# Kernel tuning notes

Measured on AMD Instinct MI355X. Metric: run time of the kernel, lower is better.

Reference implementation:

```python
import jax, jax.numpy as jnp
import numpy as np

B, C, IMG, P = 16, 3, 224, 16
L, H, D, DK, DV, M, NC = 4, 12, 768, 768, 768, 3072, 4
N = (IMG // P) ** 2  # 196 patches
S = N + 1            # +CLS
EPS = 1e-5


def _ln_stats(x):
    mu = jnp.mean(x, axis=-1, keepdims=True)
    var = jnp.var(x, axis=-1, keepdims=True)
    return (x - mu) * jax.lax.rsqrt(var + EPS)


def setup_inputs() -> dict:
    key = jax.random.key(0)
    ks = iter(jax.random.split(key, 32))
    g = lambda shape, s=0.02: jax.random.normal(next(ks), shape, jnp.float32) * s
    inp = {
        "x": jax.random.normal(next(ks), (B, C, IMG, IMG), jnp.float32),
        "W_patch": g((D, C, P, P)),
        "b_patch": jnp.zeros((D,), jnp.float32),
        "cls_tok": g((1, 1, D), 1.0),
        "pos_emb": g((1, S, D), 1.0),
        # per-layer stacked params (leading dim L); per-head LN + per-head full-width QKV
        "ln1_g": jnp.ones((L, H, D), jnp.float32),
        "ln1_b": jnp.zeros((L, H, D), jnp.float32),
        "Wq": g((L, H, D, DK)), "bq": jnp.zeros((L, H, DK), jnp.float32),
        "Wk": g((L, H, D, DK)), "bk": jnp.zeros((L, H, DK), jnp.float32),
        "Wv": g((L, H, D, DV)), "bv": jnp.zeros((L, H, DV), jnp.float32),
        "Wo": g((L, H * DK, D)), "bo": jnp.zeros((L, D), jnp.float32),
        "ln2_g": jnp.ones((L, D), jnp.float32),
        "ln2_b": jnp.zeros((L, D), jnp.float32),
        "W1": g((L, D, M)), "b1": jnp.zeros((L, M), jnp.float32),
        "W2": g((L, M, D)), "b2": jnp.zeros((L, D), jnp.float32),
        "lnf_g": jnp.ones((D,), jnp.float32),
        "lnf_b": jnp.zeros((D,), jnp.float32),
        "Wc": g((D, NC)), "bc": jnp.zeros((NC,), jnp.float32),
    }
    return inp


def _vit_forward(x, W_patch, b_patch, cls_tok, pos_emb,
                 ln1_g, ln1_b, Wq, bq, Wk, bk, Wv, bv, Wo, bo,
                 ln2_g, ln2_b, W1, b1, W2, b2, lnf_g, lnf_b, Wc, bc):
    b = x.shape[0]
    hp = IMG // P
    # patch embed: stride==kernel conv as a reshape+einsum; order matches conv flatten (h-major)
    xp = x.reshape(b, C, hp, P, hp, P)
    h = jnp.einsum('bchpwq,dcpq->bhwd', xp, W_patch).reshape(b, N, D) + b_patch
    h = jnp.concatenate([jnp.broadcast_to(cls_tok, (b, 1, D)), h], axis=1) + pos_emb

    scale = jnp.sqrt(jnp.asarray(DK, h.dtype))

    def block(h, p):
        (g1, b1_, wq, bq_, wk, bk_, wv, bv_, wo, bo_, g2, b2_, w1, bb1, w2, bb2) = p
        xn = _ln_stats(h)                                   # [B,S,D] shared stats
        xh = xn[:, None] * g1[None, :, None, :] + b1_[None, :, None, :]  # [B,H,S,D]
        q = jnp.einsum('bhsd,hdk->bhsk', xh, wq) + bq_[None, :, None, :]
        k = jnp.einsum('bhsd,hdk->bhsk', xh, wk) + bk_[None, :, None, :]
        v = jnp.einsum('bhsd,hdk->bhsk', xh, wv) + bv_[None, :, None, :]
        scores = jnp.einsum('bhqd,bhkd->bhqk', q, k) / scale
        probs = jax.nn.softmax(scores, axis=-2)             # quirk: softmax over QUERY axis
        av = jnp.einsum('bhqk,bhkd->bhqd', probs, v)        # [B,H,S,DV]
        cat = jnp.transpose(av, (0, 2, 1, 3)).reshape(b, S, H * DV)
        h = h + cat @ wo + bo_
        xn2 = _ln_stats(h) * g2 + b2_
        hid = jax.nn.gelu(xn2 @ w1 + bb1, approximate=False)
        h = h + hid @ w2 + bb2
        return h, None

    params = (ln1_g, ln1_b, Wq, bq, Wk, bk, Wv, bv, Wo, bo,
              ln2_g, ln2_b, W1, b1, W2, b2)
    h, _ = jax.lax.scan(block, h, params)
    cls = _ln_stats(h[:, 0]) * lnf_g + lnf_b
    return cls @ Wc + bc


def reference(x, W_patch, b_patch, cls_tok, pos_emb,
              ln1_g, ln1_b, Wq, bq, Wk, bk, Wv, bv, Wo, bo,
              ln2_g, ln2_b, W1, b1, W2, b2, lnf_g, lnf_b, Wc, bc):
    return _vit_forward(x, W_patch, b_patch, cls_tok, pos_emb,
                        ln1_g, ln1_b, Wq, bq, Wk, bk, Wv, bv, Wo, bo,
                        ln2_g, ln2_b, W1, b1, W2, b2, lnf_g, lnf_b, Wc, bc)
```

## Files before the change

### kernel.cpp

```cpp
#include <hip/hip_runtime.h>
#include <hip/hip_bf16.h>
#include <math.h>

typedef float f32x4 __attribute__((ext_vector_type(4)));
typedef __bf16 bf16x8 __attribute__((ext_vector_type(8)));

#define EPI_PATCH  0
#define EPI_QKV    1
#define EPI_SCORES 2
#define EPI_AV     3
#define EPI_GELU   4
#define EPI_RESID  5

template<int EPI>
__global__ __launch_bounds__(256)
void gemm_bt(const __hip_bfloat16* __restrict__ Ag,
             const __hip_bfloat16* __restrict__ Bg,
             const int M, const int N, const int K,
             const int lda, const int ldb,
             const long sA, const long sB,
             void* __restrict__ outv,
             const float* __restrict__ bias,
             const float* __restrict__ bias2,
             const int ldo, const float p1)
{
    __shared__ unsigned short As[128][32];
    __shared__ unsigned short Bs[128][32];
    const int tid  = threadIdx.x;
    const int lane = tid & 63;
    const int wave = tid >> 6;
    const int wm = (wave & 1) << 6;
    const int wn = (wave >> 1) << 6;
    const int m0 = blockIdx.y * 128;
    const int n0 = blockIdx.x * 128;
    const int z  = blockIdx.z;
    const __hip_bfloat16* A = Ag + (size_t)z * sA;
    const __hip_bfloat16* B = Bg + (size_t)z * sB;

    f32x4 acc[4][4] = {};

    const int fr = lane & 15;
    const int q8 = (lane >> 4) << 3;
    const int rr = tid >> 2;
    const int kc = (tid & 3) << 3;

    for (int k0 = 0; k0 < K; k0 += 32) {
        #pragma unroll
        for (int i = 0; i < 2; ++i) {
            const int r = rr + (i << 6);
            int ra = m0 + r; ra = (ra < M) ? ra : (M - 1);
            int rb = n0 + r; rb = (rb < N) ? rb : (N - 1);
            const uint4 va = *(const uint4*)(A + (size_t)ra * lda + (k0 + kc));
            const uint4 vb = *(const uint4*)(B + (size_t)rb * ldb + (k0 + kc));
            *(uint4*)(&As[r][kc]) = va;
            *(uint4*)(&Bs[r][kc]) = vb;
        }
        __syncthreads();
        bf16x8 af[4], bfr[4];
        #pragma unroll
        for (int mi = 0; mi < 4; ++mi) {
            af[mi] = *(const bf16x8*)(&As[wm + (mi << 4) + fr][q8]);
        }
        #pragma unroll
        for (int ni = 0; ni < 4; ++ni) {
            bfr[ni] = *(const bf16x8*)(&Bs[wn + (ni << 4) + fr][q8]);
        }
        #pragma unroll
        for (int mi = 0; mi < 4; ++mi) {
            #pragma unroll
            for (int ni = 0; ni < 4; ++ni) {
                acc[mi][ni] = __builtin_amdgcn_mfma_f32_16x16x32_bf16(
                    af[mi], bfr[ni], acc[mi][ni], 0, 0, 0);
            }
        }
        __syncthreads();
    }

    const int q4 = (lane >> 4) << 2;
    #pragma unroll
    for (int mi = 0; mi < 4; ++mi) {
        #pragma unroll
        for (int ni = 0; ni < 4; ++ni) {
            #pragma unroll
            for (int r = 0; r < 4; ++r) {
                const int m = m0 + wm + (mi << 4) + q4 + r;
                const int n = n0 + wn + (ni << 4) + fr;
                if (m < M && n < N) {
                    const float v = acc[mi][ni][r];
                    if (EPI == EPI_PATCH) {
                        float* h = (float*)outv;
                        const int b = m / 196;
                        const int pp = m - b * 196;
                        h[(size_t)(m + b + 1) * 768 + n] =
                            v + bias[n] + bias2[(size_t)(1 + pp) * 768 + n];
                    } else if (EPI == EPI_QKV) {
                        __hip_bfloat16* o = (__hip_bfloat16*)outv;
                        const int b = m / 197, s = m - b * 197;
                        const int hh = n / 768, kq = n - hh * 768;
                        o[((size_t)((b * 12 + hh) * 197 + s)) * 768 + kq] =
                            __float2bfloat16(v + bias[n]);
                    } else if (EPI == EPI_SCORES) {
                        float* o = (float*)outv + (size_t)z * 38809;
                        o[(size_t)m * 197 + n] = v * p1;
                    } else if (EPI == EPI_AV) {
                        __hip_bfloat16* o = (__hip_bfloat16*)outv;
                        const int b = z / 12, hh = z - b * 12;
                        o[(size_t)b * 197 * 9216 + (size_t)m * 9216 + hh * 768 + n] =
                            __float2bfloat16(v);
                    } else if (EPI == EPI_GELU) {
                        __hip_bfloat16* o = (__hip_bfloat16*)outv;
                        const float t = v + bias[n];
                        o[(size_t)m * ldo + n] =
                            __float2bfloat16(0.5f * t * (1.0f + erff(t * 0.70710678118654752f)));
                    } else if (EPI == EPI_RESID) {
                        float* h = (float*)outv;
                        h[(size_t)m * 768 + n] += v + bias[n];
                    }
                }
            }
        }
    }
}

__global__ __launch_bounds__(256)
void ln_rows(const float* __restrict__ h, __hip_bfloat16* __restrict__ xn)
{
    const int r = blockIdx.x;
    const float* x = h + (size_t)r * 768;
    float v[3]; float s = 0.f, sq = 0.f;
    #pragma unroll
    for (int i = 0; i < 3; ++i) {
        v[i] = x[threadIdx.x + i * 256];
        s += v[i]; sq += v[i] * v[i];
    }
    __shared__ float sb[8];
    #pragma unroll
    for (int off = 32; off; off >>= 1) {
        s += __shfl_down(s, off); sq += __shfl_down(sq, off);
    }
    const int w = threadIdx.x >> 6;
    if ((threadIdx.x & 63) == 0) { sb[w] = s; sb[4 + w] = sq; }
    __syncthreads();
    s = sb[0] + sb[1] + sb[2] + sb[3];
    sq = sb[4] + sb[5] + sb[6] + sb[7];
    const float mu = s * (1.f / 768.f);
    const float var = sq * (1.f / 768.f) - mu * mu;
    const float rstd = rsqrtf(var + 1e-5f);
    __hip_bfloat16* o = xn + (size_t)r * 768;
    #pragma unroll
    for (int i = 0; i < 3; ++i) {
        o[threadIdx.x + i * 256] = __float2bfloat16((v[i] - mu) * rstd);
    }
}

__global__ __launch_bounds__(256)
void softmax_q(const float* __restrict__ scores, __hip_bfloat16* __restrict__ probs)
{
    const int z = blockIdx.x;
    const float* sc = scores + (size_t)z * 38809;
    __hip_bfloat16* pr = probs + (size_t)z * 197 * 224;
    const int k = threadIdx.x;
    if (k >= 224) return;
    if (k < 197) {
        float mx = -1e30f;
        for (int q = 0; q < 197; ++q) mx = fmaxf(mx, sc[(size_t)q * 197 + k]);
        float sum = 0.f;
        for (int q = 0; q < 197; ++q) sum += expf(sc[(size_t)q * 197 + k] - mx);
        const float inv = 1.f / sum;
        for (int q = 0; q < 197; ++q) {
            pr[(size_t)q * 224 + k] =
                __float2bfloat16(expf(sc[(size_t)q * 197 + k] - mx) * inv);
        }
    } else {
        const __hip_bfloat16 zz = __float2bfloat16(0.f);
        for (int q = 0; q < 197; ++q) pr[(size_t)q * 224 + k] = zz;
    }
}

__device__ __forceinline__
void tconv_body(const float* __restrict__ src, __hip_bfloat16* __restrict__ dst,
                const int R, const int C,
                const float* __restrict__ gain, const float* __restrict__ bvec,
                float* __restrict__ bias_out, const int r0, const int c0)
{
    __shared__ float tile[32][33];
    __shared__ float pb[8][32];
    const int tx = threadIdx.x & 31, ty = threadIdx.x >> 5;
    float bacc = 0.f;
    #pragma unroll
    for (int i = 0; i < 4; ++i) {
        const int r = r0 + ty + i * 8;
        const float w = src[(size_t)r * C + c0 + tx];
        tile[ty + i * 8][tx] = w * (gain ? gain[r] : 1.f);
        if (bvec) bacc += bvec[r] * w;
    }
    if (bias_out) pb[ty][tx] = bacc;
    __syncthreads();
    #pragma unroll
    for (int i = 0; i < 4; ++i) {
        const int c = c0 + ty + i * 8;
        dst[(size_t)c * R + r0 + tx] = __float2bfloat16(tile[tx][ty + i * 8]);
    }
    if (bias_out && ty == 0) {
        float sum = 0.f;
        #pragma unroll
        for (int j = 0; j < 8; ++j) sum += pb[j][tx];
        atomicAdd(&bias_out[c0 + tx], sum);
    }
}

__global__ __launch_bounds__(256)
void tconv_plain(const float* __restrict__ src, __hip_bfloat16* __restrict__ dst,
                 const int R, const int C, const float* __restrict__ gain,
                 const float* __restrict__ bvec, float* __restrict__ bias_out)
{
    tconv_body(src, dst, R, C, gain, bvec, bias_out, blockIdx.y * 32, blockIdx.x * 32);
}

__global__ __launch_bounds__(256)
void tconv_qkv(const float* __restrict__ Wq, const float* __restrict__ Wk,
               const float* __restrict__ Wv, const float* __restrict__ g1,
               const float* __restrict__ b1, __hip_bfloat16* __restrict__ dst,
               float* __restrict__ bias_out, const int l)
{
    const int zz = blockIdx.z;
    const int proj = zz / 12, hh = zz - proj * 12;
    const float* W = (proj == 0) ? Wq : ((proj == 1) ? Wk : Wv);
    const float* src = W + (size_t)(l * 12 + hh) * 768 * 768;
    const float* g = g1 + (size_t)(l * 12 + hh) * 768;
    const float* bv = b1 + (size_t)(l * 12 + hh) * 768;
    __hip_bfloat16* d = dst + ((size_t)proj * 9216 + (size_t)hh * 768) * 768;
    float* bo = bias_out + proj * 9216 + hh * 768;
    tconv_body(src, d, 768, 768, g, bv, bo, blockIdx.y * 32, blockIdx.x * 32);
}

__global__ __launch_bounds__(256)
void vtrans(const __hip_bfloat16* __restrict__ v, __hip_bfloat16* __restrict__ vt)
{
    const int z = blockIdx.z;
    const __hip_bfloat16* src = v + (size_t)z * 197 * 768;
    __hip_bfloat16* dst = vt + (size_t)z * 768 * 224;
    __shared__ __hip_bfloat16 tile[32][33];
    const int tx = threadIdx.x & 31, ty = threadIdx.x >> 5;
    const int s0 = blockIdx.y * 32, d0 = blockIdx.x * 32;
    #pragma unroll
    for (int i = 0; i < 4; ++i) {
        const int s = s0 + ty + i * 8;
        tile[ty + i * 8][tx] = (s < 197) ? src[(size_t)s * 768 + d0 + tx]
                                         : __float2bfloat16(0.f);
    }
    __syncthreads();
    #pragma unroll
    for (int i = 0; i < 4; ++i) {
        const int d = d0 + ty + i * 8;
        dst[(size_t)d * 224 + s0 + tx] = tile[tx][ty + i * 8];
    }
}

__global__ void im2col_patch(const float* __restrict__ x, __hip_bfloat16* __restrict__ Ap)
{
    const int idx = blockIdx.x * 256 + threadIdx.x;
    if (idx >= 3136 * 768) return;
    const int m = idx / 768, kk = idx - m * 768;
    const int b = m / 196, pidx = m - b * 196;
    const int ph = pidx / 14, pw = pidx - ph * 14;
    const int c = kk >> 8, rrr = kk & 255;
    const int p = rrr >> 4, q = rrr & 15;
    Ap[idx] = __float2bfloat16(
        x[(((size_t)b * 3 + c) * 224 + ph * 16 + p) * 224 + pw * 16 + q]);
}

__global__ void conv_ew(const float* __restrict__ src, __hip_bfloat16* __restrict__ dst, const int n)
{
    const int i = blockIdx.x * 256 + threadIdx.x;
    if (i < n) dst[i] = __float2bfloat16(src[i]);
}

__global__ void cls_pos(const float* __restrict__ cls, const float* __restrict__ pos,
                        float* __restrict__ h)
{
    const int i = blockIdx.x * 256 + threadIdx.x;
    if (i < 16 * 768) {
        const int b = i / 768, d = i - b * 768;
        h[(size_t)b * 197 * 768 + d] = cls[d] + pos[d];
    }
}

__global__ void binit_qkv(const float* __restrict__ bq, const float* __restrict__ bk,
                          const float* __restrict__ bv, float* __restrict__ bias, const int l)
{
    const int n = blockIdx.x * 256 + threadIdx.x;
    if (n < 3 * 9216) {
        const int proj = n / 9216, rem = n - proj * 9216;
        const int hh = rem / 768, kq = rem - hh * 768;
        const float* src = (proj == 0) ? bq : ((proj == 1) ? bk : bv);
        bias[n] = src[(size_t)(l * 12 + hh) * 768 + kq];
    }
}

__global__ void binit_vec(const float* __restrict__ src, float* __restrict__ dst, const int n)
{
    const int i = blockIdx.x * 256 + threadIdx.x;
    if (i < n) dst[i] = src[i];
}

__global__ __launch_bounds__(256)
void final_head(const float* __restrict__ h, const float* __restrict__ lnfg,
                const float* __restrict__ lnfb, const float* __restrict__ Wc,
                const float* __restrict__ bc, float* __restrict__ out)
{
    const int b = blockIdx.x;
    const float* x = h + (size_t)b * 197 * 768;
    float v[3]; float s = 0.f, sq = 0.f;
    #pragma unroll
    for (int i = 0; i < 3; ++i) {
        v[i] = x[threadIdx.x + i * 256];
        s += v[i]; sq += v[i] * v[i];
    }
    __shared__ float sb[8];
    #pragma unroll
    for (int off = 32; off; off >>= 1) {
        s += __shfl_down(s, off); sq += __shfl_down(sq, off);
    }
    const int w = threadIdx.x >> 6;
    if ((threadIdx.x & 63) == 0) { sb[w] = s; sb[4 + w] = sq; }
    __syncthreads();
    s = sb[0] + sb[1] + sb[2] + sb[3];
    sq = sb[4] + sb[5] + sb[6] + sb[7];
    const float mu = s * (1.f / 768.f);
    const float var = sq * (1.f / 768.f) - mu * mu;
    const float rstd = rsqrtf(var + 1e-5f);
    float pacc[4] = {0.f, 0.f, 0.f, 0.f};
    #pragma unroll
    for (int i = 0; i < 3; ++i) {
        const int d = threadIdx.x + i * 256;
        const float c = (v[i] - mu) * rstd * lnfg[d] + lnfb[d];
        #pragma unroll
        for (int n = 0; n < 4; ++n) pacc[n] += c * Wc[d * 4 + n];
    }
    __shared__ float rb[4][4];
    #pragma unroll
    for (int off = 32; off; off >>= 1) {
        #pragma unroll
        for (int n = 0; n < 4; ++n) pacc[n] += __shfl_down(pacc[n], off);
    }
    if ((threadIdx.x & 63) == 0) {
        #pragma unroll
        for (int n = 0; n < 4; ++n) rb[w][n] = pacc[n];
    }
    __syncthreads();
    if (threadIdx.x < 4) {
        out[b * 4 + threadIdx.x] =
            rb[0][threadIdx.x] + rb[1][threadIdx.x] + rb[2][threadIdx.x] +
            rb[3][threadIdx.x] + bc[threadIdx.x];
    }
}

extern "C" void kernel_launch(void* const* d_in, const int* in_sizes, int n_in,
                              void* d_out, int out_size, void* d_ws, size_t ws_size,
                              hipStream_t stream)
{
    const float* x    = (const float*)d_in[0];
    const float* Wp   = (const float*)d_in[1];
    const float* bp   = (const float*)d_in[2];
    const float* cls  = (const float*)d_in[3];
    const float* pos  = (const float*)d_in[4];
    const float* g1   = (const float*)d_in[5];
    const float* b1v  = (const float*)d_in[6];
    const float* Wq   = (const float*)d_in[7];
    const float* bq   = (const float*)d_in[8];
    const float* Wk   = (const float*)d_in[9];
    const float* bk   = (const float*)d_in[10];
    const float* Wv   = (const float*)d_in[11];
    const float* bv   = (const float*)d_in[12];
    const float* Wo   = (const float*)d_in[13];
    const float* bo   = (const float*)d_in[14];
    const float* g2   = (const float*)d_in[15];
    const float* b2v  = (const float*)d_in[16];
    const float* W1   = (const float*)d_in[17];
    const float* bb1  = (const float*)d_in[18];
    const float* W2   = (const float*)d_in[19];
    const float* bb2  = (const float*)d_in[20];
    const float* lnfg = (const float*)d_in[21];
    const float* lnfb = (const float*)d_in[22];
    const float* Wc   = (const float*)d_in[23];
    const float* bc   = (const float*)d_in[24];
    float* out = (float*)d_out;

    char* p = (char*)d_ws;
    auto alloc = [&](size_t bytes) {
        char* r = p; p += (bytes + 255) & ~(size_t)255; return r;
    };
    float*          h       = (float*)         alloc((size_t)3152 * 768 * 4);
    __hip_bfloat16* xn      = (__hip_bfloat16*)alloc((size_t)3152 * 768 * 2);
    __hip_bfloat16* Ap      = (__hip_bfloat16*)alloc((size_t)3136 * 768 * 2);
    __hip_bfloat16* Wpb     = (__hip_bfloat16*)alloc((size_t)768 * 768 * 2);
    __hip_bfloat16* Wqkvl   = (__hip_bfloat16*)alloc((size_t)3 * 9216 * 768 * 2);
    float*          biasqkv = (float*)         alloc((size_t)3 * 9216 * 4);
    __hip_bfloat16* Wol     = (__hip_bfloat16*)alloc((size_t)768 * 9216 * 2);
    __hip_bfloat16* W1l     = (__hip_bfloat16*)alloc((size_t)3072 * 768 * 2);
    float*          bias1   = (float*)         alloc((size_t)3072 * 4);
    __hip_bfloat16* W2l     = (__hip_bfloat16*)alloc((size_t)768 * 3072 * 2);
    __hip_bfloat16* qb      = (__hip_bfloat16*)alloc((size_t)192 * 197 * 768 * 2);
    __hip_bfloat16* kb      = (__hip_bfloat16*)alloc((size_t)192 * 197 * 768 * 2);
    __hip_bfloat16* vb      = (__hip_bfloat16*)alloc((size_t)192 * 197 * 768 * 2);
    __hip_bfloat16* vt      = (__hip_bfloat16*)alloc((size_t)192 * 768 * 224 * 2);
    float*          sc      = (float*)         alloc((size_t)192 * 197 * 197 * 4);
    __hip_bfloat16* pr      = (__hip_bfloat16*)alloc((size_t)192 * 197 * 224 * 2);
    __hip_bfloat16* cat     = (__hip_bfloat16*)alloc((size_t)3152 * 9216 * 2);
    __hip_bfloat16* hid     = (__hip_bfloat16*)alloc((size_t)3152 * 3072 * 2);
    (void)in_sizes; (void)n_in; (void)out_size; (void)ws_size;

    conv_ew<<<(768 * 768 + 255) / 256, 256, 0, stream>>>(Wp, Wpb, 768 * 768);
    im2col_patch<<<(3136 * 768 + 255) / 256, 256, 0, stream>>>(x, Ap);
    cls_pos<<<(16 * 768 + 255) / 256, 256, 0, stream>>>(cls, pos, h);
    gemm_bt<EPI_PATCH><<<dim3(6, 25, 1), 256, 0, stream>>>(
        Ap, Wpb, 3136, 768, 768, 768, 768, 0, 0, h, bp, pos, 768, 0.f);

    const float sinv = 0.036084391824351615f;

    for (int l = 0; l < 4; ++l) {
        binit_qkv<<<(27648 + 255) / 256, 256, 0, stream>>>(bq, bk, bv, biasqkv, l);
        tconv_qkv<<<dim3(24, 24, 36), 256, 0, stream>>>(Wq, Wk, Wv, g1, b1v, Wqkvl, biasqkv, l);
        tconv_plain<<<dim3(24, 288, 1), 256, 0, stream>>>(
            Wo + (size_t)l * 9216 * 768, Wol, 9216, 768, nullptr, nullptr, nullptr);
        binit_vec<<<(3072 + 255) / 256, 256, 0, stream>>>(bb1 + (size_t)l * 3072, bias1, 3072);
        tconv_plain<<<dim3(96, 24, 1), 256, 0, stream>>>(
            W1 + (size_t)l * 768 * 3072, W1l, 768, 3072, g2 + l * 768, b2v + l * 768, bias1);
        tconv_plain<<<dim3(24, 96, 1), 256, 0, stream>>>(
            W2 + (size_t)l * 3072 * 768, W2l, 3072, 768, nullptr, nullptr, nullptr);

        ln_rows<<<3152, 256, 0, stream>>>(h, xn);
        gemm_bt<EPI_QKV><<<dim3(72, 25, 1), 256, 0, stream>>>(
            xn, Wqkvl, 3152, 9216, 768, 768, 768, 0, 0, qb, biasqkv, nullptr, 0, 0.f);
        gemm_bt<EPI_QKV><<<dim3(72, 25, 1), 256, 0, stream>>>(
            xn, Wqkvl + (size_t)9216 * 768, 3152, 9216, 768, 768, 768, 0, 0,
            kb, biasqkv + 9216, nullptr, 0, 0.f);
        gemm_bt<EPI_QKV><<<dim3(72, 25, 1), 256, 0, stream>>>(
            xn, Wqkvl + (size_t)2 * 9216 * 768, 3152, 9216, 768, 768, 768, 0, 0,
            vb, biasqkv + 2 * 9216, nullptr, 0, 0.f);
        vtrans<<<dim3(24, 7, 192), 256, 0, stream>>>(vb, vt);
        gemm_bt<EPI_SCORES><<<dim3(2, 2, 192), 256, 0, stream>>>(
            qb, kb, 197, 197, 768, 768, 768, (long)197 * 768, (long)197 * 768,
            sc, nullptr, nullptr, 197, sinv);
        softmax_q<<<192, 256, 0, stream>>>(sc, pr);
        gemm_bt<EPI_AV><<<dim3(6, 2, 192), 256, 0, stream>>>(
            pr, vt, 197, 768, 224, 224, 224, (long)197 * 224, (long)768 * 224,
            cat, nullptr, nullptr, 0, 0.f);
        gemm_bt<EPI_RESID><<<dim3(6, 25, 1), 256, 0, stream>>>(
            cat, Wol, 3152, 768, 9216, 9216, 9216, 0, 0, h, bo + l * 768, nullptr, 768, 0.f);

        ln_rows<<<3152, 256, 0, stream>>>(h, xn);
        gemm_bt<EPI_GELU><<<dim3(24, 25, 1), 256, 0, stream>>>(
            xn, W1l, 3152, 3072, 768, 768, 768, 0, 0, hid, bias1, nullptr, 3072, 0.f);
        gemm_bt<EPI_RESID><<<dim3(6, 25, 1), 256, 0, stream>>>(
            hid, W2l, 3152, 768, 3072, 3072, 3072, 0, 0, h, bb2 + l * 768, nullptr, 768, 0.f);
    }

    final_head<<<16, 256, 0, stream>>>(h, lnfg, lnfb, Wc, bc, out);
}
```

Baseline: 4.354 ms.

## Use direct global-to-LDS loads, split-K atomics, and fused QKV GEMM

The GEMM tile loader now uses global_load_lds with an XOR swizzle on the k-column, so data goes straight into shared memory and LDS bank conflicts drop. The narrow N=768 GEMMs (patch embed, output projection, FFN down) are split along K across blockIdx.z and combined with float atomicAdd, which raises the block count from 150. The bias and position-embedding terms move into a full h initialisation kernel. The three Q/K/V GEMMs merge into one launch over 27648 columns. Atomics add contention and make the summation order nondeterministic.

```diff
diff --git a/kernel.cpp b/kernel.cpp
--- a/kernel.cpp
+++ b/kernel.cpp
@@ -12,7 +12,13 @@
 #define EPI_GELU   4
 #define EPI_RESID  5
 
-template<int EPI>
+__device__ __forceinline__ void gld16(const void* g, void* l) {
+    __builtin_amdgcn_global_load_lds(
+        (const __attribute__((address_space(1))) unsigned int*)g,
+        (__attribute__((address_space(3))) unsigned int*)l, 16, 0, 0);
+}
+
+template<int EPI, bool SPLIT>
 __global__ __launch_bounds__(256)
 void gemm_bt(const __hip_bfloat16* __restrict__ Ag,
              const __hip_bfloat16* __restrict__ Bg,
@@ -21,8 +27,7 @@
              const long sA, const long sB,
              void* __restrict__ outv,
              const float* __restrict__ bias,
-             const float* __restrict__ bias2,
-             const int ldo, const float p1)
+             const int ldo, const float p1, const int Kc)
 {
     __shared__ unsigned short As[128][32];
     __shared__ unsigned short Bs[128][32];
@@ -39,40 +44,36 @@
 
     f32x4 acc[4][4] = {};
 
-    const int fr = lane & 15;
-    const int q8 = (lane >> 4) << 3;
-    const int rr = tid >> 2;
-    const int kc = (tid & 3) << 3;
-
-    for (int k0 = 0; k0 < K; k0 += 32) {
+    const int fr  = lane & 15;
+    const int rr  = tid >> 2;
+    const int ksw = (((tid & 3) ^ ((tid >> 3) & 3)) << 3);
+    const int colX = (((lane >> 4) ^ ((fr >> 1) & 3)) << 3);
+
+    int kBeg = 0, kEnd = K;
+    if (SPLIT) { kBeg = z * Kc; kEnd = (kBeg + Kc < K) ? (kBeg + Kc) : K; }
+
+    for (int k0 = kBeg; k0 < kEnd; k0 += 32) {
         #pragma unroll
         for (int i = 0; i < 2; ++i) {
-            const int r = rr + (i << 6);
-            int ra = m0 + r; ra = (ra < M) ? ra : (M - 1);
-            int rb = n0 + r; rb = (rb < N) ? rb : (N - 1);
-            const uint4 va = *(const uint4*)(A + (size_t)ra * lda + (k0 + kc));
-            const uint4 vb = *(const uint4*)(B + (size_t)rb * ldb + (k0 + kc));
-            *(uint4*)(&As[r][kc]) = va;
-            *(uint4*)(&Bs[r][kc]) = vb;
+            int ra = m0 + rr + (i << 6); ra = (ra < M) ? ra : (M - 1);
+            int rb = n0 + rr + (i << 6); rb = (rb < N) ? rb : (N - 1);
+            gld16(A + (size_t)ra * lda + (k0 + ksw), &As[(wave << 4) + (i << 6)][0]);
+            gld16(B + (size_t)rb * ldb + (k0 + ksw), &Bs[(wave << 4) + (i << 6)][0]);
         }
         __syncthreads();
         bf16x8 af[4], bfr[4];
         #pragma unroll
-        for (int mi = 0; mi < 4; ++mi) {
-            af[mi] = *(const bf16x8*)(&As[wm + (mi << 4) + fr][q8]);
-        }
-        #pragma unroll
-        for (int ni = 0; ni < 4; ++ni) {
-            bfr[ni] = *(const bf16x8*)(&Bs[wn + (ni << 4) + fr][q8]);
-        }
-        #pragma unroll
-        for (int mi = 0; mi < 4; ++mi) {
+        for (int mi = 0; mi < 4; ++mi)
+            af[mi] = *(const bf16x8*)(&As[wm + (mi << 4) + fr][colX]);
+        #pragma unroll
+        for (int ni = 0; ni < 4; ++ni)
+            bfr[ni] = *(const bf16x8*)(&Bs[wn + (ni << 4) + fr][colX]);
+        #pragma unroll
+        for (int mi = 0; mi < 4; ++mi)
             #pragma unroll
-            for (int ni = 0; ni < 4; ++ni) {
+            for (int ni = 0; ni < 4; ++ni)
                 acc[mi][ni] = __builtin_amdgcn_mfma_f32_16x16x32_bf16(
                     af[mi], bfr[ni], acc[mi][ni], 0, 0, 0);
-            }
-        }
         __syncthreads();
     }
 
@@ -90,14 +91,14 @@
                     if (EPI == EPI_PATCH) {
                         float* h = (float*)outv;
                         const int b = m / 196;
-                        const int pp = m - b * 196;
-                        h[(size_t)(m + b + 1) * 768 + n] =
-                            v + bias[n] + bias2[(size_t)(1 + pp) * 768 + n];
+                        atomicAdd(&h[(size_t)(m + b + 1) * 768 + n], v);
                     } else if (EPI == EPI_QKV) {
                         __hip_bfloat16* o = (__hip_bfloat16*)outv;
                         const int b = m / 197, s = m - b * 197;
-                        const int hh = n / 768, kq = n - hh * 768;
-                        o[((size_t)((b * 12 + hh) * 197 + s)) * 768 + kq] =
+                        const int proj = n / 9216, rem = n - proj * 9216;
+                        const int hh = rem / 768, kq = rem - hh * 768;
+                        o[(size_t)proj * 29048832 +
+                          ((size_t)((b * 12 + hh) * 197 + s)) * 768 + kq] =
                             __float2bfloat16(v + bias[n]);
                     } else if (EPI == EPI_SCORES) {
                         float* o = (float*)outv + (size_t)z * 38809;
@@ -114,7 +115,12 @@
                             __float2bfloat16(0.5f * t * (1.0f + erff(t * 0.70710678118654752f)));
                     } else if (EPI == EPI_RESID) {
                         float* h = (float*)outv;
-                        h[(size_t)m * 768 + n] += v + bias[n];
+                        if (SPLIT) {
+                            atomicAdd(&h[(size_t)m * 768 + n],
+                                      v + ((z == 0) ? bias[n] : 0.f));
+                        } else {
+                            h[(size_t)m * 768 + n] += v + bias[n];
+                        }
                     }
                 }
             }
@@ -148,9 +154,8 @@
     const float rstd = rsqrtf(var + 1e-5f);
     __hip_bfloat16* o = xn + (size_t)r * 768;
     #pragma unroll
-    for (int i = 0; i < 3; ++i) {
+    for (int i = 0; i < 3; ++i)
         o[threadIdx.x + i * 256] = __float2bfloat16((v[i] - mu) * rstd);
-    }
 }
 
 __global__ __launch_bounds__(256)
@@ -167,10 +172,9 @@
         float sum = 0.f;
         for (int q = 0; q < 197; ++q) sum += expf(sc[(size_t)q * 197 + k] - mx);
         const float inv = 1.f / sum;
-        for (int q = 0; q < 197; ++q) {
+        for (int q = 0; q < 197; ++q)
             pr[(size_t)q * 224 + k] =
                 __float2bfloat16(expf(sc[(size_t)q * 197 + k] - mx) * inv);
-        }
     } else {
         const __hip_bfloat16 zz = __float2bfloat16(0.f);
         for (int q = 0; q < 197; ++q) pr[(size_t)q * 224 + k] = zz;
@@ -276,13 +280,14 @@
     if (i < n) dst[i] = __float2bfloat16(src[i]);
 }
 
-__global__ void cls_pos(const float* __restrict__ cls, const float* __restrict__ pos,
-                        float* __restrict__ h)
+__global__ void hinit(const float* __restrict__ cls, const float* __restrict__ pos,
+                      const float* __restrict__ bp, float* __restrict__ h)
 {
     const int i = blockIdx.x * 256 + threadIdx.x;
-    if (i < 16 * 768) {
-        const int b = i / 768, d = i - b * 768;
-        h[(size_t)b * 197 * 768 + d] = cls[d] + pos[d];
+    if (i < 16 * 197 * 768) {
+        const int rem = i % (197 * 768);
+        const int s = rem / 768, d = rem - s * 768;
+        h[i] = pos[rem] + ((s == 0) ? cls[d] : bp[d]);
     }
 }
 
@@ -340,20 +345,17 @@
     }
     __shared__ float rb[4][4];
     #pragma unroll
-    for (int off = 32; off; off >>= 1) {
+    for (int off = 32; off; off >>= 1)
         #pragma unroll
         for (int n = 0; n < 4; ++n) pacc[n] += __shfl_down(pacc[n], off);
-    }
-    if ((threadIdx.x & 63) == 0) {
+    if ((threadIdx.x & 63) == 0)
         #pragma unroll
         for (int n = 0; n < 4; ++n) rb[w][n] = pacc[n];
-    }
     __syncthreads();
-    if (threadIdx.x < 4) {
+    if (threadIdx.x < 4)
         out[b * 4 + threadIdx.x] =
             rb[0][threadIdx.x] + rb[1][threadIdx.x] + rb[2][threadIdx.x] +
             rb[3][threadIdx.x] + bc[threadIdx.x];
-    }
 }
 
 extern "C" void kernel_launch(void* const* d_in, const int* in_sizes, int n_in,
@@ -401,9 +403,9 @@
     __hip_bfloat16* W1l     = (__hip_bfloat16*)alloc((size_t)3072 * 768 * 2);
     float*          bias1   = (float*)         alloc((size_t)3072 * 4);
     __hip_bfloat16* W2l     = (__hip_bfloat16*)alloc((size_t)768 * 3072 * 2);
-    __hip_bfloat16* qb      = (__hip_bfloat16*)alloc((size_t)192 * 197 * 768 * 2);
-    __hip_bfloat16* kb      = (__hip_bfloat16*)alloc((size_t)192 * 197 * 768 * 2);
-    __hip_bfloat16* vb      = (__hip_bfloat16*)alloc((size_t)192 * 197 * 768 * 2);
+    __hip_bfloat16* qb      = (__hip_bfloat16*)alloc((size_t)3 * 29048832 * 2);
+    __hip_bfloat16* kb      = qb + (size_t)29048832;
+    __hip_bfloat16* vb      = qb + (size_t)2 * 29048832;
     __hip_bfloat16* vt      = (__hip_bfloat16*)alloc((size_t)192 * 768 * 224 * 2);
     float*          sc      = (float*)         alloc((size_t)192 * 197 * 197 * 4);
     __hip_bfloat16* pr      = (__hip_bfloat16*)alloc((size_t)192 * 197 * 224 * 2);
@@ -413,9 +415,9 @@
 
     conv_ew<<<(768 * 768 + 255) / 256, 256, 0, stream>>>(Wp, Wpb, 768 * 768);
     im2col_patch<<<(3136 * 768 + 255) / 256, 256, 0, stream>>>(x, Ap);
-    cls_pos<<<(16 * 768 + 255) / 256, 256, 0, stream>>>(cls, pos, h);
-    gemm_bt<EPI_PATCH><<<dim3(6, 25, 1), 256, 0, stream>>>(
-        Ap, Wpb, 3136, 768, 768, 768, 768, 0, 0, h, bp, pos, 768, 0.f);
+    hinit<<<(16 * 197 * 768 + 255) / 256, 256, 0, stream>>>(cls, pos, bp, h);
+    gemm_bt<EPI_PATCH, true><<<dim3(6, 25, 4), 256, 0, stream>>>(
+        Ap, Wpb, 3136, 768, 768, 768, 768, 0, 0, h, nullptr, 768, 0.f, 192);
 
     const float sinv = 0.036084391824351615f;
 
@@ -431,30 +433,24 @@
             W2 + (size_t)l * 3072 * 768, W2l, 3072, 768, nullptr, nullptr, nullptr);
 
         ln_rows<<<3152, 256, 0, stream>>>(h, xn);
-        gemm_bt<EPI_QKV><<<dim3(72, 25, 1), 256, 0, stream>>>(
-            xn, Wqkvl, 3152, 9216, 768, 768, 768, 0, 0, qb, biasqkv, nullptr, 0, 0.f);
-        gemm_bt<EPI_QKV><<<dim3(72, 25, 1), 256, 0, stream>>>(
-            xn, Wqkvl + (size_t)9216 * 768, 3152, 9216, 768, 768, 768, 0, 0,
-            kb, biasqkv + 9216, nullptr, 0, 0.f);
-        gemm_bt<EPI_QKV><<<dim3(72, 25, 1), 256, 0, stream>>>(
-            xn, Wqkvl + (size_t)2 * 9216 * 768, 3152, 9216, 768, 768, 768, 0, 0,
-            vb, biasqkv + 2 * 9216, nullptr, 0, 0.f);
+        gemm_bt<EPI_QKV, false><<<dim3(216, 25, 1), 256, 0, stream>>>(
+            xn, Wqkvl, 3152, 27648, 768, 768, 768, 0, 0, qb, biasqkv, 0, 0.f, 0);
         vtrans<<<dim3(24, 7, 192), 256, 0, stream>>>(vb, vt);
-        gemm_bt<EPI_SCORES><<<dim3(2, 2, 192), 256, 0, stream>>>(
+        gemm_bt<EPI_SCORES, false><<<dim3(2, 2, 192), 256, 0, stream>>>(
             qb, kb, 197, 197, 768, 768, 768, (long)197 * 768, (long)197 * 768,
-            sc, nullptr, nullptr, 197, sinv);
+            sc, nullptr, 197, sinv, 0);
         softmax_q<<<192, 256, 0, stream>>>(sc, pr);
-        gemm_bt<EPI_AV><<<dim3(6, 2, 192), 256, 0, stream>>>(
+        gemm_bt<EPI_AV, false><<<dim3(6, 2, 192), 256, 0, stream>>>(
             pr, vt, 197, 768, 224, 224, 224, (long)197 * 224, (long)768 * 224,
-            cat, nullptr, nullptr, 0, 0.f);
-        gemm_bt<EPI_RESID><<<dim3(6, 25, 1), 256, 0, stream>>>(
-            cat, Wol, 3152, 768, 9216, 9216, 9216, 0, 0, h, bo + l * 768, nullptr, 768, 0.f);
+            cat, nullptr, 0, 0.f, 0);
+        gemm_bt<EPI_RESID, true><<<dim3(6, 25, 6), 256, 0, stream>>>(
+            cat, Wol, 3152, 768, 9216, 9216, 9216, 0, 0, h, bo + l * 768, 768, 0.f, 1536);
 
         ln_rows<<<3152, 256, 0, stream>>>(h, xn);
-        gemm_bt<EPI_GELU><<<dim3(24, 25, 1), 256, 0, stream>>>(
-            xn, W1l, 3152, 3072, 768, 768, 768, 0, 0, hid, bias1, nullptr, 3072, 0.f);
-        gemm_bt<EPI_RESID><<<dim3(6, 25, 1), 256, 0, stream>>>(
-            hid, W2l, 3152, 768, 3072, 3072, 3072, 0, 0, h, bb2 + l * 768, nullptr, 768, 0.f);
+        gemm_bt<EPI_GELU, false><<<dim3(24, 25, 1), 256, 0, stream>>>(
+            xn, W1l, 3152, 3072, 768, 768, 768, 0, 0, hid, bias1, 3072, 0.f, 0);
+        gemm_bt<EPI_RESID, true><<<dim3(6, 25, 4), 256, 0, stream>>>(
+            hid, W2l, 3152, 768, 3072, 3072, 3072, 0, 0, h, bb2 + l * 768, 768, 0.f, 768);
     }
 
     final_head<<<16, 256, 0, stream>>>(h, lnfg, lnfb, Wc, bc, out);
```

Measured after the change: 3.661 ms. 1.19x faster.
